# Optimization experiments

Hardware: AMD Instinct MI355X
Metric: run time of the kernel (lower is better)

Reference implementation:

```python
import jax, jax.numpy as jnp
import numpy as np

B, H, W, C = 16, 64, 64, 256


def setup_inputs() -> dict:
    key = jax.random.key(0)
    k1, k2, k3 = jax.random.split(key, 3)
    x = jax.random.normal(k1, (B, H, W, C), dtype=jnp.float32)
    # 1x1 convs are channel matmuls; lecun_normal ~ N(0, 1/fan_in)
    W_qkv = jax.random.normal(k2, (C, 3 * C), dtype=jnp.float32) / np.sqrt(C)
    W_out = jax.random.normal(k3, (C, C), dtype=jnp.float32) / np.sqrt(C)
    b_out = jnp.zeros((C,), dtype=jnp.float32)
    return {"x": x, "W_qkv": W_qkv, "W_out": W_out, "b_out": b_out}


def reference(x, W_qkv, W_out, b_out):
    b, h, w, c = x.shape
    n = h * w
    # to_qkv: 1x1 conv, no bias -> channel matmul
    qkv = jnp.einsum('bhwc,cd->bhwd', x, W_qkv)            # [b,h,w,3c]
    q, k, v = jnp.split(qkv, 3, axis=-1)                    # each [b,h,w,c]
    # rearrange to [b, c, n] (heads=1)
    q = q.reshape(b, n, c).transpose(0, 2, 1)
    k = k.reshape(b, n, c).transpose(0, 2, 1)
    v = v.reshape(b, n, c).transpose(0, 2, 1)
    k = jax.nn.softmax(k, axis=-1)                          # softmax over spatial n
    context = jnp.einsum('bdn,ben->bde', k, v)              # [b,c,c] per-sample context
    out = jnp.einsum('bde,bdn->ben', context, q)            # [b,c,n]
    out = out.reshape(b, c, h, w).transpose(0, 2, 3, 1)     # [b,h,w,c]
    # to_out: 1x1 conv with bias
    return jnp.einsum('bhwc,cd->bhwd', out, W_out) + b_out
```

## Files before the change

### kernel.cpp

```cpp
#include <hip/hip_runtime.h>
#include <hip/hip_bf16.h>


typedef __bf16 bf16;
typedef __bf16 bf16x4 __attribute__((ext_vector_type(4)));
typedef __bf16 bf16x8 __attribute__((ext_vector_type(8)));
typedef float  f32x4  __attribute__((ext_vector_type(4)));

#define LDP 72

__device__ __forceinline__ bf16 tob(float f) { return (bf16)f; }

__device__ __forceinline__ void gl_lds16(const void* g, void* l) {
  __builtin_amdgcn_global_load_lds(
      (const __attribute__((address_space(1))) void*)g,
      (__attribute__((address_space(3))) void*)l, 16, 0, 0);
}

__device__ __forceinline__ void stage128x64(const bf16* __restrict__ src,
                                            size_t stride, bf16* lds, int tid) {
#pragma unroll
  for (int r = 0; r < 4; ++r) {
    int e = (r * 256 + tid) * 8;
    int row = e >> 6, col = e & 63;
    gl_lds16(src + (size_t)row * stride + col, lds + e);
  }
}

__device__ __forceinline__ void compute_tile64(const bf16* As, const bf16* Bs,
                                               f32x4 acc[4][4], int wr, int wc,
                                               int lr, int g) {
#pragma unroll
  for (int ks = 0; ks < 2; ++ks) {
    bf16x8 a[4], b[4];
#pragma unroll
    for (int m = 0; m < 4; ++m)
      a[m] = *reinterpret_cast<const bf16x8*>(&As[(wr * 64 + m * 16 + lr) * 64 + ks * 32 + g * 8]);
#pragma unroll
    for (int n = 0; n < 4; ++n)
      b[n] = *reinterpret_cast<const bf16x8*>(&Bs[(wc * 64 + n * 16 + lr) * 64 + ks * 32 + g * 8]);
#pragma unroll
    for (int m = 0; m < 4; ++m)
#pragma unroll
      for (int n = 0; n < 4; ++n)
        acc[m][n] = __builtin_amdgcn_mfma_f32_16x16x32_bf16(a[m], b[n], acc[m][n], 0, 0, 0);
  }
}

__device__ __forceinline__ void compute_tileP(const bf16* As, const bf16* Bs,
                                              f32x4 acc[4][4], int wr, int wc,
                                              int lr, int g) {
#pragma unroll
  for (int ks = 0; ks < 2; ++ks) {
    bf16x8 a[4], b[4];
#pragma unroll
    for (int m = 0; m < 4; ++m)
      a[m] = *reinterpret_cast<const bf16x8*>(&As[(wr * 64 + m * 16 + lr) * LDP + ks * 32 + g * 8]);
#pragma unroll
    for (int n = 0; n < 4; ++n)
      b[n] = *reinterpret_cast<const bf16x8*>(&Bs[(wc * 64 + n * 16 + lr) * LDP + ks * 32 + g * 8]);
#pragma unroll
    for (int m = 0; m < 4; ++m)
#pragma unroll
      for (int n = 0; n < 4; ++n)
        acc[m][n] = __builtin_amdgcn_mfma_f32_16x16x32_bf16(a[m], b[n], acc[m][n], 0, 0, 0);
  }
}

__global__ __launch_bounds__(256) void k_prep(const float* __restrict__ x,
                                              const float* __restrict__ Wq,
                                              const float* __restrict__ Wo,
                                              bf16* __restrict__ xb,
                                              bf16* __restrict__ WqT,
                                              bf16* __restrict__ WoT,
                                              float* __restrict__ S) {
  int b = blockIdx.x, tid = threadIdx.x;
  if (b < 4096) {
    size_t base = (size_t)b * 4096;
#pragma unroll
    for (int r = 0; r < 4; ++r) {
      size_t e = base + r * 1024 + tid * 4;
      float4 v = *reinterpret_cast<const float4*>(x + e);
      bf16x4 p;
      p[0] = tob(v.x); p[1] = tob(v.y); p[2] = tob(v.z); p[3] = tob(v.w);
      *reinterpret_cast<bf16x4*>(xb + e) = p;
    }
    if (b < 16) S[b * 256 + tid] = 0.0f;
  } else {
    int i0 = (b - 4096) * 1024 + tid * 4;
#pragma unroll
    for (int j = 0; j < 4; ++j) {
      int idx = i0 + j;
      if (idx < 196608) {
        int n = idx >> 8, k = idx & 255;
        WqT[idx] = tob(Wq[(size_t)k * 768 + n]);
      } else {
        int i2 = idx - 196608;
        int co = i2 >> 8, e2 = i2 & 255;
        WoT[i2] = tob(Wo[(size_t)e2 * 256 + co]);
      }
    }
  }
}

__global__ __launch_bounds__(256) void k_qkv(const bf16* __restrict__ xb,
                                             const bf16* __restrict__ WqT,
                                             bf16* __restrict__ Q,
                                             bf16* __restrict__ Et,
                                             bf16* __restrict__ Vt,
                                             float* __restrict__ S) {
  __shared__ __align__(16) bf16 As[128 * 64];
  __shared__ __align__(16) bf16 Bs[128 * 64];
  int bx = blockIdx.x;
  int swz = (bx & 7) * 384 + (bx >> 3);
  int rb = swz / 6, cb = swz % 6;
  int tid = threadIdx.x;
  int lane = tid & 63, w = tid >> 6;
  int wr = w >> 1, wc = w & 1;
  int g = lane >> 4, lr = lane & 15;
  const int rowbase = rb * 128, colbase = cb * 128;

  f32x4 acc[4][4];
#pragma unroll
  for (int m = 0; m < 4; ++m)
#pragma unroll
    for (int n = 0; n < 4; ++n) acc[m][n] = (f32x4)0.0f;

  for (int kt = 0; kt < 4; ++kt) {
    int k0 = kt * 64;
    __syncthreads();
    stage128x64(xb + (size_t)rowbase * 256 + k0, 256, As, tid);
    stage128x64(WqT + (size_t)colbase * 256 + k0, 256, Bs, tid);
    __syncthreads();
    compute_tile64(As, Bs, acc, wr, wc, lr, g);
  }

  int grow = rowbase + wr * 64;
  int gcol = colbase + wc * 64;
  int sec = gcol >> 8;
  int coff = gcol & 255;
  int b = grow >> 12;
  int nsp = grow & 4095;

  if (sec == 0) {
#pragma unroll
    for (int m = 0; m < 4; ++m)
#pragma unroll
      for (int n = 0; n < 4; ++n) {
        int col = coff + n * 16 + lr;
#pragma unroll
        for (int t = 0; t < 4; ++t) {
          int row = grow + m * 16 + g * 4 + t;
          Q[(size_t)row * 256 + col] = tob(acc[m][n][t]);
        }
      }
  } else {
    bf16* dst = (sec == 1) ? Et : Vt;
    float cs0 = 0.f, cs1 = 0.f, cs2 = 0.f, cs3 = 0.f;
#pragma unroll
    for (int m = 0; m < 4; ++m)
#pragma unroll
      for (int n = 0; n < 4; ++n) {
        int col = coff + n * 16 + lr;
        int nn0 = nsp + m * 16 + g * 4;
        bf16x4 p;
#pragma unroll
        for (int t = 0; t < 4; ++t) {
          float v = acc[m][n][t];
          if (sec == 1) {
            v = expf(v);
            if (n == 0) cs0 += v; else if (n == 1) cs1 += v;
            else if (n == 2) cs2 += v; else cs3 += v;
          }
          p[t] = tob(v);
        }
        *reinterpret_cast<bf16x4*>(&dst[((size_t)(b * 256 + col) << 12) + nn0]) = p;
      }
    if (sec == 1) {
      cs0 += __shfl_xor(cs0, 16); cs0 += __shfl_xor(cs0, 32);
      cs1 += __shfl_xor(cs1, 16); cs1 += __shfl_xor(cs1, 32);
      cs2 += __shfl_xor(cs2, 16); cs2 += __shfl_xor(cs2, 32);
      cs3 += __shfl_xor(cs3, 16); cs3 += __shfl_xor(cs3, 32);
      float v = (g == 0) ? cs0 : (g == 1) ? cs1 : (g == 2) ? cs2 : cs3;
      atomicAdd(&S[b * 256 + coff + g * 16 + lr], v);
    }
  }
}

__global__ __launch_bounds__(256) void k_ctx(const bf16* __restrict__ Et,
                                             const bf16* __restrict__ Vt,
                                             float* __restrict__ part) {
  __shared__ __align__(16) bf16 As[128 * 64];
  __shared__ __align__(16) bf16 Bs[128 * 64];
  int bx = blockIdx.x;
  int swz = (bx & 7) * 64 + (bx >> 3);
  int tile = swz & 3, dblk = tile >> 1, eblk = tile & 1;
  int s = (swz >> 2) & 7;
  int b = swz >> 5;
  int tid = threadIdx.x;
  int lane = tid & 63, w = tid >> 6;
  int wr = w >> 1, wc = w & 1;
  int g = lane >> 4, lr = lane & 15;

  const bf16* Ab = Et + (((size_t)(b * 256 + dblk * 128)) << 12) + s * 512;
  const bf16* Bb = Vt + (((size_t)(b * 256 + eblk * 128)) << 12) + s * 512;

  f32x4 acc[4][4];
#pragma unroll
  for (int m = 0; m < 4; ++m)
#pragma unroll
    for (int n = 0; n < 4; ++n) acc[m][n] = (f32x4)0.0f;

  for (int kt = 0; kt < 8; ++kt) {
    __syncthreads();
    stage128x64(Ab + kt * 64, 4096, As, tid);
    stage128x64(Bb + kt * 64, 4096, Bs, tid);
    __syncthreads();
    compute_tile64(As, Bs, acc, wr, wc, lr, g);
  }

  float* p = part + (size_t)(b * 8 + s) * 65536;
  int dbase = dblk * 128 + wr * 64;
  int ebase = eblk * 128 + wc * 64;
#pragma unroll
  for (int m = 0; m < 4; ++m)
#pragma unroll
    for (int n = 0; n < 4; ++n)
#pragma unroll
      for (int t = 0; t < 4; ++t)
        p[(size_t)(dbase + m * 16 + g * 4 + t) * 256 + ebase + n * 16 + lr] = acc[m][n][t];
}

__global__ __launch_bounds__(256) void k_wc(const float* __restrict__ part,
                                            const float* __restrict__ S,
                                            const bf16* __restrict__ WoT,
                                            bf16* __restrict__ WcT) {
  __shared__ __align__(16) bf16 As[128 * LDP];
  __shared__ __align__(16) bf16 Bs[128 * LDP];
  int bx = blockIdx.x;
  int b = bx >> 2, dblk = (bx >> 1) & 1, cblk = bx & 1;
  int tid = threadIdx.x;
  int lane = tid & 63, w = tid >> 6;
  int wr = w >> 1, wc = w & 1;
  int g = lane >> 4, lr = lane & 15;
  const float* p0 = part + (size_t)b * 8 * 65536;

  f32x4 acc[4][4];
#pragma unroll
  for (int m = 0; m < 4; ++m)
#pragma unroll
    for (int n = 0; n < 4; ++n) acc[m][n] = (f32x4)0.0f;

  for (int kt = 0; kt < 4; ++kt) {
    int k0 = kt * 64;
    __syncthreads();
#pragma unroll
    for (int r = 0; r < 8; ++r) {
      int idx = r * 1024 + tid * 4;
      int row = idx >> 6, col = idx & 63;
      int d = dblk * 128 + row;
      size_t off = (size_t)d * 256 + k0 + col;
      float4 a0 = *reinterpret_cast<const float4*>(p0 + off);
      float4 a1 = *reinterpret_cast<const float4*>(p0 + 65536 + off);
      float4 a2 = *reinterpret_cast<const float4*>(p0 + 2 * 65536 + off);
      float4 a3 = *reinterpret_cast<const float4*>(p0 + 3 * 65536 + off);
      float4 a4 = *reinterpret_cast<const float4*>(p0 + 4 * 65536 + off);
      float4 a5 = *reinterpret_cast<const float4*>(p0 + 5 * 65536 + off);
      float4 a6 = *reinterpret_cast<const float4*>(p0 + 6 * 65536 + off);
      float4 a7 = *reinterpret_cast<const float4*>(p0 + 7 * 65536 + off);
      float rs = 1.0f / S[b * 256 + d];
      bf16x4 p;
      p[0] = tob((a0.x + a1.x + a2.x + a3.x + a4.x + a5.x + a6.x + a7.x) * rs);
      p[1] = tob((a0.y + a1.y + a2.y + a3.y + a4.y + a5.y + a6.y + a7.y) * rs);
      p[2] = tob((a0.z + a1.z + a2.z + a3.z + a4.z + a5.z + a6.z + a7.z) * rs);
      p[3] = tob((a0.w + a1.w + a2.w + a3.w + a4.w + a5.w + a6.w + a7.w) * rs);
      *reinterpret_cast<bf16x4*>(&As[row * LDP + col]) = p;
    }
#pragma unroll
    for (int r = 0; r < 4; ++r) {
      int idx = r * 2048 + tid * 8;
      int row = idx >> 6, col = idx & 63;
      bf16x8 v = *reinterpret_cast<const bf16x8*>(WoT + (size_t)(cblk * 128 + row) * 256 + k0 + col);
      *reinterpret_cast<bf16x8*>(&Bs[row * LDP + col]) = v;
    }
    __syncthreads();
    compute_tileP(As, Bs, acc, wr, wc, lr, g);
  }

  int dbase = dblk * 128 + wr * 64;
  int cbase = cblk * 128 + wc * 64;
#pragma unroll
  for (int m = 0; m < 4; ++m)
#pragma unroll
    for (int n = 0; n < 4; ++n) {
      int co = cbase + n * 16 + lr;
      int d0 = dbase + m * 16 + g * 4;
      bf16x4 p;
#pragma unroll
      for (int t = 0; t < 4; ++t) p[t] = tob(acc[m][n][t]);
      *reinterpret_cast<bf16x4*>(&WcT[(size_t)b * 65536 + (size_t)co * 256 + d0]) = p;
    }
}

__global__ __launch_bounds__(256) void k_out(const bf16* __restrict__ Q,
                                             const bf16* __restrict__ WcT,
                                             const float* __restrict__ b_out,
                                             float* __restrict__ y) {
  __shared__ __align__(16) bf16 As[128 * 64];
  __shared__ __align__(16) bf16 Bs[128 * 64];
  int bx = blockIdx.x;
  int swz = (bx & 7) * 128 + (bx >> 3);
  int rb = swz >> 1, cbk = swz & 1;
  int tid = threadIdx.x;
  int lane = tid & 63, w = tid >> 6;
  int wr = w >> 1, wc = w & 1;
  int g = lane >> 4, lr = lane & 15;
  int rowbase = rb * 128;
  int b = rowbase >> 12;
  const bf16* Bb = WcT + (size_t)b * 65536;

  f32x4 acc[4][4];
#pragma unroll
  for (int m = 0; m < 4; ++m)
#pragma unroll
    for (int n = 0; n < 4; ++n) acc[m][n] = (f32x4)0.0f;

  for (int kt = 0; kt < 4; ++kt) {
    int k0 = kt * 64;
    __syncthreads();
    stage128x64(Q + (size_t)rowbase * 256 + k0, 256, As, tid);
    stage128x64(Bb + (size_t)(cbk * 128) * 256 + k0, 256, Bs, tid);
    __syncthreads();
    compute_tile64(As, Bs, acc, wr, wc, lr, g);
  }

  int cbase = cbk * 128 + wc * 64;
#pragma unroll
  for (int m = 0; m < 4; ++m)
#pragma unroll
    for (int n = 0; n < 4; ++n) {
      int col = cbase + n * 16 + lr;
      float bo = b_out[col];
#pragma unroll
      for (int t = 0; t < 4; ++t) {
        int row = rowbase + wr * 64 + m * 16 + g * 4 + t;
        y[(size_t)row * 256 + col] = acc[m][n][t] + bo;
      }
    }
}

extern "C" void kernel_launch(void* const* d_in, const int* in_sizes, int n_in,
                              void* d_out, int out_size, void* d_ws, size_t ws_size,
                              hipStream_t stream) {
  (void)in_sizes; (void)n_in; (void)out_size; (void)ws_size;
  const float* x  = (const float*)d_in[0];
  const float* Wq = (const float*)d_in[1];
  const float* Wo = (const float*)d_in[2];
  const float* bo = (const float*)d_in[3];
  float* y = (float*)d_out;

  char* ws = (char*)d_ws;
  bf16*  Q    = (bf16*)(ws);
  bf16*  Et   = (bf16*)(ws + 33554432);
  bf16*  Vt   = (bf16*)(ws + 67108864);
  bf16*  xb   = (bf16*)(ws + 100663296);
  float* part = (float*)(ws + 100663296);
  bf16*  WcT  = (bf16*)(ws + 134217728);
  bf16*  WqT  = (bf16*)(ws + 136314880);
  bf16*  WoT  = (bf16*)(ws + 136708096);
  float* S    = (float*)(ws + 136839168);

  k_prep<<<dim3(4352), dim3(256), 0, stream>>>(x, Wq, Wo, xb, WqT, WoT, S);
  k_qkv<<<dim3(3072), dim3(256), 0, stream>>>(xb, WqT, Q, Et, Vt, S);
  k_ctx<<<dim3(512), dim3(256), 0, stream>>>(Et, Vt, part);
  k_wc<<<dim3(64), dim3(256), 0, stream>>>(part, S, WoT, WcT);
  k_out<<<dim3(1024), dim3(256), 0, stream>>>(Q, WcT, bo, y);
}
```

Baseline: 247.1 us.

## Double-buffer LDS tiles and XOR-swizzle layout in GEMM kernels

```diff
diff --git a/kernel.cpp b/kernel.cpp
--- a/kernel.cpp
+++ b/kernel.cpp
@@ -17,28 +17,30 @@
       (__attribute__((address_space(3))) void*)l, 16, 0, 0);
 }
 
-__device__ __forceinline__ void stage128x64(const bf16* __restrict__ src,
-                                            size_t stride, bf16* lds, int tid) {
+__device__ __forceinline__ void stage_swz(const bf16* __restrict__ src,
+                                          size_t stride, bf16* lds, int tid) {
 #pragma unroll
   for (int r = 0; r < 4; ++r) {
-    int e = (r * 256 + tid) * 8;
-    int row = e >> 6, col = e & 63;
-    gl_lds16(src + (size_t)row * stride + col, lds + e);
-  }
-}
-
-__device__ __forceinline__ void compute_tile64(const bf16* As, const bf16* Bs,
-                                               f32x4 acc[4][4], int wr, int wc,
-                                               int lr, int g) {
+    int si = r * 256 + tid;
+    int row = si >> 3, c16 = si & 7;
+    int gcol = (c16 ^ (row & 7)) << 3;
+    gl_lds16(src + (size_t)row * stride + gcol, lds + si * 8);
+  }
+}
+
+__device__ __forceinline__ void compute_tile_swz(const bf16* As, const bf16* Bs,
+                                                 f32x4 acc[4][4], int wr, int wc,
+                                                 int lr, int g) {
 #pragma unroll
   for (int ks = 0; ks < 2; ++ks) {
+    int slot = ((ks * 4 + g) ^ (lr & 7)) * 8;
     bf16x8 a[4], b[4];
 #pragma unroll
     for (int m = 0; m < 4; ++m)
-      a[m] = *reinterpret_cast<const bf16x8*>(&As[(wr * 64 + m * 16 + lr) * 64 + ks * 32 + g * 8]);
+      a[m] = *reinterpret_cast<const bf16x8*>(&As[(wr * 64 + m * 16 + lr) * 64 + slot]);
 #pragma unroll
     for (int n = 0; n < 4; ++n)
-      b[n] = *reinterpret_cast<const bf16x8*>(&Bs[(wc * 64 + n * 16 + lr) * 64 + ks * 32 + g * 8]);
+      b[n] = *reinterpret_cast<const bf16x8*>(&Bs[(wc * 64 + n * 16 + lr) * 64 + slot]);
 #pragma unroll
     for (int m = 0; m < 4; ++m)
 #pragma unroll
@@ -109,8 +111,7 @@
                                              bf16* __restrict__ Et,
                                              bf16* __restrict__ Vt,
                                              float* __restrict__ S) {
-  __shared__ __align__(16) bf16 As[128 * 64];
-  __shared__ __align__(16) bf16 Bs[128 * 64];
+  __shared__ __align__(16) bf16 As0[8192], Bs0[8192], As1[8192], Bs1[8192];
   int bx = blockIdx.x;
   int swz = (bx & 7) * 384 + (bx >> 3);
   int rb = swz / 6, cb = swz % 6;
@@ -119,6 +120,8 @@
   int wr = w >> 1, wc = w & 1;
   int g = lane >> 4, lr = lane & 15;
   const int rowbase = rb * 128, colbase = cb * 128;
+  const bf16* Ab = xb + (size_t)rowbase * 256;
+  const bf16* Bb = WqT + (size_t)colbase * 256;
 
   f32x4 acc[4][4];
 #pragma unroll
@@ -126,13 +129,22 @@
 #pragma unroll
     for (int n = 0; n < 4; ++n) acc[m][n] = (f32x4)0.0f;
 
-  for (int kt = 0; kt < 4; ++kt) {
-    int k0 = kt * 64;
+  stage_swz(Ab, 256, As0, tid);
+  stage_swz(Bb, 256, Bs0, tid);
+  __syncthreads();
+#pragma unroll
+  for (int kp = 0; kp < 2; ++kp) {
+    int kt = kp * 2;
+    stage_swz(Ab + (kt + 1) * 64, 256, As1, tid);
+    stage_swz(Bb + (kt + 1) * 64, 256, Bs1, tid);
+    compute_tile_swz(As0, Bs0, acc, wr, wc, lr, g);
     __syncthreads();
-    stage128x64(xb + (size_t)rowbase * 256 + k0, 256, As, tid);
-    stage128x64(WqT + (size_t)colbase * 256 + k0, 256, Bs, tid);
-    __syncthreads();
-    compute_tile64(As, Bs, acc, wr, wc, lr, g);
+    if (kt + 2 < 4) {
+      stage_swz(Ab + (kt + 2) * 64, 256, As0, tid);
+      stage_swz(Bb + (kt + 2) * 64, 256, Bs0, tid);
+    }
+    compute_tile_swz(As1, Bs1, acc, wr, wc, lr, g);
+    if (kt + 2 < 4) __syncthreads();
   }
 
   int grow = rowbase + wr * 64;
@@ -190,8 +202,7 @@
 __global__ __launch_bounds__(256) void k_ctx(const bf16* __restrict__ Et,
                                              const bf16* __restrict__ Vt,
                                              float* __restrict__ part) {
-  __shared__ __align__(16) bf16 As[128 * 64];
-  __shared__ __align__(16) bf16 Bs[128 * 64];
+  __shared__ __align__(16) bf16 As0[8192], Bs0[8192], As1[8192], Bs1[8192];
   int bx = blockIdx.x;
   int swz = (bx & 7) * 64 + (bx >> 3);
   int tile = swz & 3, dblk = tile >> 1, eblk = tile & 1;
@@ -211,12 +222,22 @@
 #pragma unroll
     for (int n = 0; n < 4; ++n) acc[m][n] = (f32x4)0.0f;
 
-  for (int kt = 0; kt < 8; ++kt) {
+  stage_swz(Ab, 4096, As0, tid);
+  stage_swz(Bb, 4096, Bs0, tid);
+  __syncthreads();
+#pragma unroll
+  for (int kp = 0; kp < 4; ++kp) {
+    int kt = kp * 2;
+    stage_swz(Ab + (kt + 1) * 64, 4096, As1, tid);
+    stage_swz(Bb + (kt + 1) * 64, 4096, Bs1, tid);
+    compute_tile_swz(As0, Bs0, acc, wr, wc, lr, g);
     __syncthreads();
-    stage128x64(Ab + kt * 64, 4096, As, tid);
-    stage128x64(Bb + kt * 64, 4096, Bs, tid);
-    __syncthreads();
-    compute_tile64(As, Bs, acc, wr, wc, lr, g);
+    if (kt + 2 < 8) {
+      stage_swz(Ab + (kt + 2) * 64, 4096, As0, tid);
+      stage_swz(Bb + (kt + 2) * 64, 4096, Bs0, tid);
+    }
+    compute_tile_swz(As1, Bs1, acc, wr, wc, lr, g);
+    if (kt + 2 < 8) __syncthreads();
   }
 
   float* p = part + (size_t)(b * 8 + s) * 65536;
@@ -306,8 +327,7 @@
                                              const bf16* __restrict__ WcT,
                                              const float* __restrict__ b_out,
                                              float* __restrict__ y) {
-  __shared__ __align__(16) bf16 As[128 * 64];
-  __shared__ __align__(16) bf16 Bs[128 * 64];
+  __shared__ __align__(16) bf16 As0[8192], Bs0[8192], As1[8192], Bs1[8192];
   int bx = blockIdx.x;
   int swz = (bx & 7) * 128 + (bx >> 3);
   int rb = swz >> 1, cbk = swz & 1;
@@ -317,7 +337,8 @@
   int g = lane >> 4, lr = lane & 15;
   int rowbase = rb * 128;
   int b = rowbase >> 12;
-  const bf16* Bb = WcT + (size_t)b * 65536;
+  const bf16* Ab = Q + (size_t)rowbase * 256;
+  const bf16* Bb = WcT + (size_t)b * 65536 + (size_t)(cbk * 128) * 256;
 
   f32x4 acc[4][4];
 #pragma unroll
@@ -325,13 +346,22 @@
 #pragma unroll
     for (int n = 0; n < 4; ++n) acc[m][n] = (f32x4)0.0f;
 
-  for (int kt = 0; kt < 4; ++kt) {
-    int k0 = kt * 64;
+  stage_swz(Ab, 256, As0, tid);
+  stage_swz(Bb, 256, Bs0, tid);
+  __syncthreads();
+#pragma unroll
+  for (int kp = 0; kp < 2; ++kp) {
+    int kt = kp * 2;
+    stage_swz(Ab + (kt + 1) * 64, 256, As1, tid);
+    stage_swz(Bb + (kt + 1) * 64, 256, Bs1, tid);
+    compute_tile_swz(As0, Bs0, acc, wr, wc, lr, g);
     __syncthreads();
-    stage128x64(Q + (size_t)rowbase * 256 + k0, 256, As, tid);
-    stage128x64(Bb + (size_t)(cbk * 128) * 256 + k0, 256, Bs, tid);
-    __syncthreads();
-    compute_tile64(As, Bs, acc, wr, wc, lr, g);
+    if (kt + 2 < 4) {
+      stage_swz(Ab + (kt + 2) * 64, 256, As0, tid);
+      stage_swz(Bb + (kt + 2) * 64, 256, Bs0, tid);
+    }
+    compute_tile_swz(As1, Bs1, acc, wr, wc, lr, g);
+    if (kt + 2 < 4) __syncthreads();
   }
 
   int cbase = cbk * 128 + wc * 64;
```

Result: faster. 232.6 us (-5.9%).
